# Kernel tuning notes

Measured on AMD Instinct MI355X. Metric: run time of the kernel, lower is better.

The kernel has to match this reference:

```python
import jax, jax.numpy as jnp
import numpy as np

HEAD_DEPTH = 64
CLIP = 10.0
SCALE = float(np.sqrt(HEAD_DEPTH))


def setup_inputs() -> dict:
    key = jax.random.key(0)
    kq, kk, kv, km = jax.random.split(key, 4)
    B, H, S, D = 4, 16, 2048, HEAD_DEPTH
    q = jax.random.normal(kq, (B, H, S, D), dtype=jnp.float32)
    k = jax.random.normal(kk, (B, H, S, D), dtype=jnp.float32)
    v = jax.random.normal(kv, (B, H, S, D), dtype=jnp.float32)
    # mask: (batch, n_nodes, 1) bool; True => key position is masked out
    mask = jax.random.randint(km, (B, S, 1), 0, 2).astype(bool)
    return {"q": q, "k": k, "v": v, "mask": mask}


def reference(q, k, v, mask):
    # logits: (B, H, Sq, Sk)
    logits = jnp.einsum('bhqd,bhkd->bhqk', q, k) / SCALE
    logits = CLIP * jnp.tanh(logits)  # tanh-clip of logits
    # mask (B, N, 1) -> broadcast over heads and query positions: (B, 1, 1, N)
    key_mask = mask[:, None, None, :, 0]
    logits = jnp.where(key_mask, -jnp.inf, logits)
    probs = jax.nn.softmax(logits, axis=-1)
    return jnp.einsum('bhqk,bhkd->bhqd', probs, v)
```

## Files before the change

### kernel.cpp

```cpp
#include <hip/hip_runtime.h>

typedef short bf16x8 __attribute__((ext_vector_type(8), may_alias));
typedef float f32x4 __attribute__((ext_vector_type(4)));
typedef unsigned int u32x4a __attribute__((ext_vector_type(4), may_alias));
typedef unsigned int u32x2a __attribute__((ext_vector_type(2), may_alias));
typedef unsigned short ushort;
typedef unsigned int uint;

#define B_N 4
#define H_N 16
#define S_N 2048
#define D_N 64
#define BQ 128
#define WQ 32
#define KT 64
#define NW 4
#define NBLK (B_N*H_N*(S_N/BQ))
#define TILE_BYTES 32768
#define MAXTILE (S_N/KT)
#define IMG_OFF 32768
#define WS_NEED ((size_t)IMG_OFF + (size_t)B_N*H_N*MAXTILE*TILE_BYTES)

#define MFMA16 __builtin_amdgcn_mfma_f32_16x16x32_bf16

__device__ __forceinline__ uint f2bf(float x){
  uint u = __float_as_uint(x);
  u += 0x7fffu + ((u >> 16) & 1u);
  return u >> 16;
}
__device__ __forceinline__ float bf2f(uint h){
  return __uint_as_float(h << 16);
}
__device__ __forceinline__ int ldsw(int off, int row){
  return off ^ ((row & 7) << 4);
}
__device__ __forceinline__ void gload16(const void* g, void* l){
  __builtin_amdgcn_global_load_lds((const uint __attribute__((address_space(1)))*)g,
                                   (uint __attribute__((address_space(3)))*)l, 16, 0, 0);
}

__global__ __launch_bounds__(256)
void compact_k(const int* __restrict__ Mg, int* __restrict__ cnt_ws,
               ushort* __restrict__ idx_ws)
{
  __shared__ int sws[NW];
  const int b = blockIdx.x;
  const int tid = threadIdx.x, lane = tid & 63, w = tid >> 6;
  const int* mb = Mg + (size_t)b * S_N;
  int kept[8]; int cl = 0; int base = tid * 8;
  #pragma unroll
  for (int i = 0; i < 8; ++i){ kept[i] = (mb[base+i] == 0); cl += kept[i]; }
  int inc = cl;
  #pragma unroll
  for (int d = 1; d < 64; d <<= 1){
    int o = __shfl_up(inc, d);
    if (lane >= d) inc += o;
  }
  if (lane == 63) sws[w] = inc;
  __syncthreads();
  int s0 = sws[0], s1 = sws[1], s2 = sws[2], s3 = sws[3];
  int wo = (w > 0 ? s0 : 0) + (w > 1 ? s1 : 0) + (w > 2 ? s2 : 0);
  int pos = wo + inc - cl;
  #pragma unroll
  for (int i = 0; i < 8; ++i){
    if (kept[i]) idx_ws[b*S_N + pos++] = (ushort)(base + i);
  }
  if (tid == 0) cnt_ws[b] = s0 + s1 + s2 + s3;
}

__global__ __launch_bounds__(256)
void stage_k(const float* __restrict__ Kg, const float* __restrict__ Vg,
             const int* __restrict__ cnt_ws, const ushort* __restrict__ idx_ws,
             char* __restrict__ img)
{
  __shared__ float Vl[64*65];
  const int bid = blockIdx.x;
  const int bh = bid >> 5;
  const int tile = bid & 31;
  const int b = bh >> 4;
  const int cnt = cnt_ws[b];
  const int ntile = (cnt + 63) >> 6;
  if (tile >= ntile) return;
  const int tid = threadIdx.x;
  char* G = img + (size_t)bid * TILE_BYTES;

  const int jrow = tid >> 2, c4 = tid & 3;
  int kk = tile*64 + jrow; if (kk >= cnt) kk = cnt - 1;
  const int sidx = idx_ws[b*S_N + kk];
  const size_t kvbase = (size_t)bh * (size_t)(S_N*D_N);
  const int sw = (jrow & 7) << 4;
  {
    const float4* Kp = (const float4*)(Kg + kvbase + (size_t)sidx*D_N) + c4*4;
    float4 k0 = Kp[0], k1 = Kp[1], k2 = Kp[2], k3 = Kp[3];
    float kv[16] = {k0.x,k0.y,k0.z,k0.w,k1.x,k1.y,k1.z,k1.w,
                    k2.x,k2.y,k2.z,k2.w,k3.x,k3.y,k3.z,k3.w};
    uint h[16], l[16];
    #pragma unroll
    for (int e = 0; e < 16; ++e){
      uint hh = f2bf(kv[e]); h[e] = hh; l[e] = f2bf(kv[e] - bf2f(hh));
    }
    char* r0 = G + jrow*128;
    char* r1 = G + 8192 + jrow*128;
    *(u32x4a*)(r0 + ((c4*32)      ^ sw)) = (u32x4a){h[0]|(h[1]<<16),  h[2]|(h[3]<<16),
                                                    h[4]|(h[5]<<16),  h[6]|(h[7]<<16)};
    *(u32x4a*)(r0 + ((c4*32 + 16) ^ sw)) = (u32x4a){h[8]|(h[9]<<16),  h[10]|(h[11]<<16),
                                                    h[12]|(h[13]<<16),h[14]|(h[15]<<16)};
    *(u32x4a*)(r1 + ((c4*32)      ^ sw)) = (u32x4a){l[0]|(l[1]<<16),  l[2]|(l[3]<<16),
                                                    l[4]|(l[5]<<16),  l[6]|(l[7]<<16)};
    *(u32x4a*)(r1 + ((c4*32 + 16) ^ sw)) = (u32x4a){l[8]|(l[9]<<16),  l[10]|(l[11]<<16),
                                                    l[12]|(l[13]<<16),l[14]|(l[15]<<16)};
  }
  {
    const float4* Vp = (const float4*)(Vg + kvbase + (size_t)sidx*D_N) + c4*4;
    float4 v0 = Vp[0], v1 = Vp[1], v2 = Vp[2], v3 = Vp[3];
    float vv[16] = {v0.x,v0.y,v0.z,v0.w,v1.x,v1.y,v1.z,v1.w,
                    v2.x,v2.y,v2.z,v2.w,v3.x,v3.y,v3.z,v3.w};
    #pragma unroll
    for (int e = 0; e < 16; ++e) Vl[jrow*65 + c4*16 + e] = vv[e];
  }
  __syncthreads();
  #pragma unroll
  for (int t = 0; t < 2; ++t){
    int idx2 = tid + t*256;
    int d = idx2 >> 3, g = idx2 & 7;
    int jb = (g ^ (d & 7)) * 8;
    uint hh[8], ll[8];
    #pragma unroll
    for (int e = 0; e < 8; ++e){
      float x = Vl[(jb+e)*65 + d];
      uint h = f2bf(x); hh[e] = h; ll[e] = f2bf(x - bf2f(h));
    }
    *(u32x4a*)(G + 16384 + d*128 + g*16) =
        (u32x4a){hh[0]|(hh[1]<<16), hh[2]|(hh[3]<<16), hh[4]|(hh[5]<<16), hh[6]|(hh[7]<<16)};
    *(u32x4a*)(G + 24576 + d*128 + g*16) =
        (u32x4a){ll[0]|(ll[1]<<16), ll[2]|(ll[3]<<16), ll[4]|(ll[5]<<16), ll[6]|(ll[7]<<16)};
  }
}

__global__ __launch_bounds__(256, 2)
void attn4_k(const float* __restrict__ Qg, const char* __restrict__ img,
             const int* __restrict__ cnt_ws, float* __restrict__ Og)
{
  __shared__ __align__(16) char smem[2][16384];
  __shared__ __align__(16) ushort Pb[NW][2][512];

  const int tid  = threadIdx.x;
  const int lane = tid & 63;
  const int w    = tid >> 6;
  const int c    = lane & 15;
  const int gi   = lane >> 4;

  int bid = blockIdx.x;
  int wg  = (bid & 7) * (NBLK/8) + (bid >> 3);
  int qt  = wg & 15;
  int bh  = wg >> 4;
  int b   = bh >> 4;

  const int cnt = cnt_ws[b];
  const int nhalf = (cnt + 31) >> 5;
  const char* Gb = img + (size_t)bh * MAXTILE * TILE_BYTES;

  auto stage = [&](int hidx, int sb){
    const char* T = Gb + (size_t)(hidx >> 1) * TILE_BYTES;
    const int h = hidx & 1;
    char* Bse = (char*)&smem[sb][0];
    if (w < 2){
      const char* src = T + w*8192 + h*4096 + lane*16;
      char* dst = Bse + w*4096;
      #pragma unroll
      for (int i = 0; i < 4; ++i) gload16(src + i*1024, dst + i*1024);
    } else {
      const int hl = w - 2;
      const char* base = T + 16384 + hl*8192;
      char* dst = Bse + 8192 + hl*4096;
      #pragma unroll
      for (int i = 0; i < 4; ++i){
        int pos = i*1024 + lane*16;
        int d = pos >> 6, p = (pos >> 4) & 3;
        int sd4 = (d & 3) ^ ((d >> 2) & 3);
        int G = (h*4 + (p ^ sd4)) ^ (d & 7);
        gload16(base + d*128 + G*16, dst + i*1024);
      }
    }
  };

  if (nhalf > 0) stage(0, 0);

  const int q0w = qt * BQ + w * WQ;
  bf16x8 qh[2][2], ql[2][2];
  {
    const float* Qbase = Qg + (size_t)bh * S_N * D_N;
    #pragma unroll
    for (int qs = 0; qs < 2; ++qs){
      const float* qr = Qbase + (size_t)(q0w + qs*16 + c) * D_N;
      #pragma unroll
      for (int ks = 0; ks < 2; ++ks){
        const float4* p4 = (const float4*)(qr + ks*32 + gi*8);
        float4 x0 = p4[0], x1 = p4[1];
        float xs[8] = {x0.x,x0.y,x0.z,x0.w,x1.x,x1.y,x1.z,x1.w};
        union { bf16x8 v; ushort u[8]; } uh, ul;
        #pragma unroll
        for (int e = 0; e < 8; ++e){
          uint h = f2bf(xs[e]);
          uh.u[e] = (ushort)h;
          ul.u[e] = (ushort)f2bf(xs[e] - bf2f(h));
        }
        qh[qs][ks] = uh.v; ql[qs][ks] = ul.v;
      }
    }
  }

  f32x4 Oa[2][4];
  #pragma unroll
  for (int i = 0; i < 2; ++i)
    #pragma unroll
    for (int jj = 0; jj < 4; ++jj)
      Oa[i][jj] = (f32x4){0.f,0.f,0.f,0.f};
  float zz[2] = {0.f, 0.f};

  char* PhB = (char*)&Pb[w][0][0];
  char* PlB = (char*)&Pb[w][1][0];
  const int swc16 = (c & 7) << 4;
  const int swc8  = (c & 7) << 3;
  const int e0 = (gi*16) ^ swc16;
  const int e1 = (64 + gi*16) ^ swc16;
  const int po0 = (gi*16) ^ swc8;
  const int po1 = (gi*16 + 8) ^ swc8;
  const int vsw = ((c & 3) ^ ((c >> 2) & 3));
  const int va  = (gi ^ vsw) << 4;

  __syncthreads();

  for (int tb = 0; tb < nhalf; ++tb){
    const int buf = tb & 1;
    if (tb + 1 < nhalf) stage(tb + 1, buf ^ 1);
    const char* Khi  = &smem[buf][0];
    const char* Klo  = Khi + 4096;
    const char* VThi = Khi + 8192;
    const char* VTlo = Khi + 12288;
    const bool lastt = (tb == nhalf - 1);

    #pragma unroll
    for (int qs = 0; qs < 2; ++qs){
      #pragma unroll
      for (int kt = 0; kt < 2; ++kt){
        int row = kt*16 + c;
        const char* krh = Khi + row*128;
        const char* krl = Klo + row*128;
        bf16x8 kh0 = *(const bf16x8*)(krh + e0);
        bf16x8 kh1 = *(const bf16x8*)(krh + e1);
        bf16x8 kl0 = *(const bf16x8*)(krl + e0);
        bf16x8 kl1 = *(const bf16x8*)(krl + e1);
        f32x4 s = (f32x4){0.f,0.f,0.f,0.f};
        s = MFMA16(kh0, qh[qs][0], s, 0,0,0);
        s = MFMA16(kh1, qh[qs][1], s, 0,0,0);
        s = MFMA16(kh0, ql[qs][0], s, 0,0,0);
        s = MFMA16(kh1, ql[qs][1], s, 0,0,0);
        s = MFMA16(kl0, qh[qs][0], s, 0,0,0);
        s = MFMA16(kl1, qh[qs][1], s, 0,0,0);
        float pv[4];
        #pragma unroll
        for (int r = 0; r < 4; ++r){
          float t  = __builtin_amdgcn_exp2f(s[r] * 0.3606737602222409f);
          float wv = __builtin_amdgcn_rcpf(t + 1.0f);
          pv[r] = __builtin_amdgcn_exp2f(-28.853900817779268f * wv);
        }
        if (lastt){
          int kg0 = tb*32 + kt*16 + gi*4;
          #pragma unroll
          for (int r = 0; r < 4; ++r) if (kg0 + r >= cnt) pv[r] = 0.f;
        }
        zz[qs] += (pv[0] + pv[1]) + (pv[2] + pv[3]);
        uint hA, hB, lA, lB;
        asm("v_cvt_pk_bf16_f32 %0, %1, %2" : "=v"(hA) : "v"(pv[0]), "v"(pv[1]));
        asm("v_cvt_pk_bf16_f32 %0, %1, %2" : "=v"(hB) : "v"(pv[2]), "v"(pv[3]));
        float l0 = pv[0] - __uint_as_float(hA << 16);
        float l1 = pv[1] - __uint_as_float(hA & 0xffff0000u);
        float l2 = pv[2] - __uint_as_float(hB << 16);
        float l3 = pv[3] - __uint_as_float(hB & 0xffff0000u);
        asm("v_cvt_pk_bf16_f32 %0, %1, %2" : "=v"(lA) : "v"(l0), "v"(l1));
        asm("v_cvt_pk_bf16_f32 %0, %1, %2" : "=v"(lB) : "v"(l2), "v"(l3));
        int ow = c*64 + ((kt*32 + gi*8) ^ swc8);
        *(u32x2a*)(PhB + ow) = (u32x2a){hA, hB};
        *(u32x2a*)(PlB + ow) = (u32x2a){lA, lB};
      }
      union PU { bf16x8 v; u32x2a g[2]; };
      PU pah, pal;
      pah.g[0] = *(const u32x2a*)(PhB + c*64 + po0);
      pah.g[1] = *(const u32x2a*)(PhB + c*64 + po1);
      pal.g[0] = *(const u32x2a*)(PlB + c*64 + po0);
      pal.g[1] = *(const u32x2a*)(PlB + c*64 + po1);
      #pragma unroll
      for (int ds = 0; ds < 4; ++ds){
        int drow = ds*16 + c;
        bf16x8 vh = *(const bf16x8*)(VThi + drow*64 + va);
        bf16x8 vl = *(const bf16x8*)(VTlo + drow*64 + va);
        f32x4 o = Oa[qs][ds];
        o = MFMA16(pah.v, vh, o, 0,0,0);
        o = MFMA16(pah.v, vl, o, 0,0,0);
        o = MFMA16(pal.v, vh, o, 0,0,0);
        Oa[qs][ds] = o;
      }
    }
    __syncthreads();
  }

  #pragma unroll
  for (int qs = 0; qs < 2; ++qs){
    float zt = zz[qs];
    zt += __shfl_xor(zt, 16);
    zt += __shfl_xor(zt, 32);
    float rz = 1.0f / zt;
    #pragma unroll
    for (int r = 0; r < 4; ++r){
      float rzq = __shfl(rz, gi*4 + r);
      size_t rowbase = ((size_t)bh * S_N + (size_t)(q0w + qs*16 + gi*4 + r)) * D_N;
      #pragma unroll
      for (int ds = 0; ds < 4; ++ds){
        Og[rowbase + ds*16 + c] = Oa[qs][ds][r] * rzq;
      }
    }
  }
}

__global__ __launch_bounds__(256, 2)
void attn_k(const float* __restrict__ Qg, const float* __restrict__ Kg,
            const float* __restrict__ Vg, const int* __restrict__ Mg,
            float* __restrict__ Og)
{
  __shared__ __align__(16) ushort Khi[KT*D_N];
  __shared__ __align__(16) ushort Klo[KT*D_N];
  __shared__ __align__(16) ushort Vhi[D_N*72];
  __shared__ __align__(16) ushort Vlo[D_N*72];
  __shared__ __align__(16) ushort Phl[NW*16*72];
  __shared__ __align__(16) ushort Pll[NW*16*72];
  __shared__ ushort idx_l[S_N];
  __shared__ int scan_ws[NW];

  const int tid  = threadIdx.x;
  const int lane = tid & 63;
  const int w    = tid >> 6;
  const int c    = lane & 15;
  const int gi   = lane >> 4;

  int bid = blockIdx.x;
  int wg  = (bid & 7) * (NBLK/8) + (bid >> 3);
  int qt  = wg & 15;
  int bh  = wg >> 4;
  int b   = bh >> 4;

  int cnt;
  {
    const int* mb = Mg + (size_t)b * S_N;
    int kept[8]; int cl = 0;
    int base = tid * 8;
    #pragma unroll
    for (int i = 0; i < 8; ++i){ kept[i] = (mb[base+i] == 0); cl += kept[i]; }
    int inc = cl;
    #pragma unroll
    for (int d = 1; d < 64; d <<= 1){
      int o = __shfl_up(inc, d);
      if (lane >= d) inc += o;
    }
    if (lane == 63) scan_ws[w] = inc;
    __syncthreads();
    int s0 = scan_ws[0], s1 = scan_ws[1], s2 = scan_ws[2], s3 = scan_ws[3];
    int wo = (w > 0 ? s0 : 0) + (w > 1 ? s1 : 0) + (w > 2 ? s2 : 0);
    cnt = s0 + s1 + s2 + s3;
    int pos = wo + inc - cl;
    #pragma unroll
    for (int i = 0; i < 8; ++i){
      if (kept[i]) idx_l[pos++] = (ushort)(base + i);
    }
    __syncthreads();
  }

  const int q0w = qt * BQ + w * WQ;
  bf16x8 qh[2][2], ql[2][2];
  {
    const float* Qbase = Qg + (size_t)bh * S_N * D_N;
    #pragma unroll
    for (int qs = 0; qs < 2; ++qs){
      const float* qr = Qbase + (size_t)(q0w + qs*16 + c) * D_N;
      #pragma unroll
      for (int ks = 0; ks < 2; ++ks){
        const float4* p4 = (const float4*)(qr + ks*32 + gi*8);
        float4 x0 = p4[0], x1 = p4[1];
        float xs[8] = {x0.x,x0.y,x0.z,x0.w,x1.x,x1.y,x1.z,x1.w};
        union { bf16x8 v; ushort u[8]; } uh, ul;
        #pragma unroll
        for (int e = 0; e < 8; ++e){
          uint h = f2bf(xs[e]);
          uh.u[e] = (ushort)h;
          ul.u[e] = (ushort)f2bf(xs[e] - bf2f(h));
        }
        qh[qs][ks] = uh.v; ql[qs][ks] = ul.v;
      }
    }
  }

  f32x4 Oa[2][4];
  #pragma unroll
  for (int i = 0; i < 2; ++i)
    #pragma unroll
    for (int jj = 0; jj < 4; ++jj)
      Oa[i][jj] = (f32x4){0.f,0.f,0.f,0.f};
  float zz[2] = {0.f, 0.f};

  ushort* Ph = Phl + w * (16*72);
  ushort* Pl = Pll + w * (16*72);

  const int jrow = tid >> 2;
  const int c4   = tid & 3;
  const size_t kvbase = (size_t)bh * S_N * D_N;

  const int ntile = (cnt + KT - 1) >> 6;
  for (int tb = 0; tb < ntile; ++tb){
    {
      int kk = tb*KT + jrow;
      int ci = kk < cnt ? kk : cnt - 1;
      int sidx = idx_l[ci];
      const float4* Kp = (const float4*)(Kg + kvbase + (size_t)sidx * D_N) + c4*4;
      const float4* Vp = (const float4*)(Vg + kvbase + (size_t)sidx * D_N) + c4*4;
      float4 k0 = Kp[0], k1 = Kp[1], k2 = Kp[2], k3 = Kp[3];
      float kv[16] = {k0.x,k0.y,k0.z,k0.w,k1.x,k1.y,k1.z,k1.w,
                      k2.x,k2.y,k2.z,k2.w,k3.x,k3.y,k3.z,k3.w};
      uint kh[16], klv[16];
      #pragma unroll
      for (int e = 0; e < 16; ++e){
        uint h = f2bf(kv[e]);
        kh[e] = h; klv[e] = f2bf(kv[e] - bf2f(h));
      }
      u32x4a H0 = (u32x4a){kh[0]|(kh[1]<<16),   kh[2]|(kh[3]<<16),
                           kh[4]|(kh[5]<<16),   kh[6]|(kh[7]<<16)};
      u32x4a H1 = (u32x4a){kh[8]|(kh[9]<<16),   kh[10]|(kh[11]<<16),
                           kh[12]|(kh[13]<<16), kh[14]|(kh[15]<<16)};
      u32x4a L0 = (u32x4a){klv[0]|(klv[1]<<16),   klv[2]|(klv[3]<<16),
                           klv[4]|(klv[5]<<16),   klv[6]|(klv[7]<<16)};
      u32x4a L1 = (u32x4a){klv[8]|(klv[9]<<16),   klv[10]|(klv[11]<<16),
                           klv[12]|(klv[13]<<16), klv[14]|(klv[15]<<16)};
      char* krh = (char*)Khi + jrow*128;
      char* krl = (char*)Klo + jrow*128;
      int o0 = ldsw(c4*32, jrow), o1 = ldsw(c4*32 + 16, jrow);
      *(u32x4a*)(krh + o0) = H0;  *(u32x4a*)(krh + o1) = H1;
      *(u32x4a*)(krl + o0) = L0;  *(u32x4a*)(krl + o1) = L1;

      float4 v0 = Vp[0], v1 = Vp[1], v2 = Vp[2], v3 = Vp[3];
      float vv[16] = {v0.x,v0.y,v0.z,v0.w,v1.x,v1.y,v1.z,v1.w,
                      v2.x,v2.y,v2.z,v2.w,v3.x,v3.y,v3.z,v3.w};
      #pragma unroll
      for (int e = 0; e < 16; ++e){
        int d = c4*16 + e;
        uint h  = f2bf(vv[e]);
        uint l2 = f2bf(vv[e] - bf2f(h));
        int off = d*144 + ldsw(jrow*2, d);
        *(ushort*)((char*)Vhi + off) = (ushort)h;
        *(ushort*)((char*)Vlo + off) = (ushort)l2;
      }
    }
    __syncthreads();

    const bool lastt = (tb == ntile - 1);
    #pragma unroll
    for (int qs = 0; qs < 2; ++qs){
      #pragma unroll
      for (int kt = 0; kt < 4; ++kt){
        int row = kt*16 + c;
        const char* krh = (const char*)Khi + row*128;
        const char* krl = (const char*)Klo + row*128;
        int e0 = ldsw(16*gi, row), e1 = ldsw(64 + 16*gi, row);
        bf16x8 kh0 = *(const bf16x8*)(krh + e0);
        bf16x8 kh1 = *(const bf16x8*)(krh + e1);
        bf16x8 kl0 = *(const bf16x8*)(krl + e0);
        bf16x8 kl1 = *(const bf16x8*)(krl + e1);
        f32x4 s = (f32x4){0.f,0.f,0.f,0.f};
        s = MFMA16(kh0, qh[qs][0], s, 0,0,0);
        s = MFMA16(kh1, qh[qs][1], s, 0,0,0);
        s = MFMA16(kh0, ql[qs][0], s, 0,0,0);
        s = MFMA16(kh1, ql[qs][1], s, 0,0,0);
        s = MFMA16(kl0, qh[qs][0], s, 0,0,0);
        s = MFMA16(kl1, qh[qs][1], s, 0,0,0);
        float pv[4];
        #pragma unroll
        for (int r = 0; r < 4; ++r){
          float t  = __builtin_amdgcn_exp2f(s[r] * 0.3606737602222409f);
          float wv = __builtin_amdgcn_rcpf(t + 1.0f);
          pv[r] = __builtin_amdgcn_exp2f(-28.853900817779268f * wv);
        }
        if (lastt){
          int kg0 = tb*KT + kt*16 + gi*4;
          #pragma unroll
          for (int r = 0; r < 4; ++r) if (kg0 + r >= cnt) pv[r] = 0.f;
        }
        zz[qs] += (pv[0] + pv[1]) + (pv[2] + pv[3]);
        uint h0 = f2bf(pv[0]), h1 = f2bf(pv[1]),
             h2 = f2bf(pv[2]), h3 = f2bf(pv[3]);
        uint l0 = f2bf(pv[0]-bf2f(h0)), l1 = f2bf(pv[1]-bf2f(h1)),
             l2 = f2bf(pv[2]-bf2f(h2)), l3 = f2bf(pv[3]-bf2f(h3));
        int ow = c*144 + ldsw(kt*32 + gi*8, c);
        *(u32x2a*)((char*)Ph + ow) = (u32x2a){h0|(h1<<16), h2|(h3<<16)};
        *(u32x2a*)((char*)Pl + ow) = (u32x2a){l0|(l1<<16), l2|(l3<<16)};
      }
      bf16x8 pah[2], pal[2];
      {
        const char* prh = (const char*)Ph + c*144;
        const char* prl = (const char*)Pl + c*144;
        #pragma unroll
        for (int ks = 0; ks < 2; ++ks){
          int oo = ldsw(64*ks + 16*gi, c);
          pah[ks] = *(const bf16x8*)(prh + oo);
          pal[ks] = *(const bf16x8*)(prl + oo);
        }
      }
      #pragma unroll
      for (int ds = 0; ds < 4; ++ds){
        int drow = ds*16 + c;
        const char* vrh = (const char*)Vhi + drow*144;
        const char* vrl = (const char*)Vlo + drow*144;
        f32x4 o = Oa[qs][ds];
        #pragma unroll
        for (int ks = 0; ks < 2; ++ks){
          int oo = ldsw(64*ks + 16*gi, drow);
          bf16x8 vh = *(const bf16x8*)(vrh + oo);
          bf16x8 vl = *(const bf16x8*)(vrl + oo);
          o = MFMA16(pah[ks], vh, o, 0,0,0);
          o = MFMA16(pah[ks], vl, o, 0,0,0);
          o = MFMA16(pal[ks], vh, o, 0,0,0);
        }
        Oa[qs][ds] = o;
      }
    }
    __syncthreads();
  }

  #pragma unroll
  for (int qs = 0; qs < 2; ++qs){
    float zt = zz[qs];
    zt += __shfl_xor(zt, 16);
    zt += __shfl_xor(zt, 32);
    float rz = 1.0f / zt;
    #pragma unroll
    for (int r = 0; r < 4; ++r){
      float rzq = __shfl(rz, gi*4 + r);
      size_t rowbase = ((size_t)bh * S_N + (size_t)(q0w + qs*16 + gi*4 + r)) * D_N;
      #pragma unroll
      for (int ds = 0; ds < 4; ++ds){
        Og[rowbase + ds*16 + c] = Oa[qs][ds][r] * rzq;
      }
    }
  }
}

extern "C" void kernel_launch(void* const* d_in, const int* in_sizes, int n_in,
                              void* d_out, int out_size, void* d_ws, size_t ws_size,
                              hipStream_t stream) {
  const float* Qg = (const float*)d_in[0];
  const float* Kg = (const float*)d_in[1];
  const float* Vg = (const float*)d_in[2];
  const int*   Mg = (const int*)d_in[3];
  float* Og = (float*)d_out;
  if (ws_size >= WS_NEED){
    int*    cnt_ws = (int*)d_ws;
    ushort* idx_ws = (ushort*)((char*)d_ws + 64);
    char*   img    = (char*)d_ws + IMG_OFF;
    compact_k<<<dim3(B_N), dim3(256), 0, stream>>>(Mg, cnt_ws, idx_ws);
    stage_k<<<dim3(B_N*H_N*MAXTILE), dim3(256), 0, stream>>>(Kg, Vg, cnt_ws, idx_ws, img);
    attn4_k<<<dim3(NBLK), dim3(256), 0, stream>>>(Qg, img, cnt_ws, Og);
  } else {
    attn_k<<<dim3(NBLK), dim3(256), 0, stream>>>(Qg, Kg, Vg, Mg, Og);
  }
}
```

Measured before the change: 157.1 us.

## Keep softmax probabilities in registers by permuting V layout to match MFMA output

The V transpose image in the staging kernel is reordered so that the key index permutation matches the MFMA accumulator layout. The attention kernel can then feed the packed bf16 probabilities straight from registers as the A operand of the PV MFMA, skipping the per-warp LDS round trip for P. The loops are also reordered so K fragments load once for both query subtiles and V fragments load once for both. The cost is more live registers, which could pressure occupancy at two blocks per CU, and the V swizzle is dropped, which may bring back LDS bank conflicts.

```diff
diff --git a/kernel.cpp b/kernel.cpp
--- a/kernel.cpp
+++ b/kernel.cpp
@@ -122,27 +122,29 @@
   #pragma unroll
   for (int t = 0; t < 2; ++t){
     int idx2 = tid + t*256;
-    int d = idx2 >> 3, g = idx2 & 7;
-    int jb = (g ^ (d & 7)) * 8;
+    int d = idx2 >> 3;
+    int h = (idx2 >> 2) & 1;
+    int g = idx2 & 3;
+    int kb = h*32 + g*4;
     uint hh[8], ll[8];
     #pragma unroll
     for (int e = 0; e < 8; ++e){
-      float x = Vl[(jb+e)*65 + d];
-      uint h = f2bf(x); hh[e] = h; ll[e] = f2bf(x - bf2f(h));
-    }
-    *(u32x4a*)(G + 16384 + d*128 + g*16) =
+      int k = kb + (e & 3) + ((e >> 2) << 4);
+      float x = Vl[k*65 + d];
+      uint hv = f2bf(x); hh[e] = hv; ll[e] = f2bf(x - bf2f(hv));
+    }
+    *(u32x4a*)(G + 16384 + d*128 + h*64 + g*16) =
         (u32x4a){hh[0]|(hh[1]<<16), hh[2]|(hh[3]<<16), hh[4]|(hh[5]<<16), hh[6]|(hh[7]<<16)};
-    *(u32x4a*)(G + 24576 + d*128 + g*16) =
+    *(u32x4a*)(G + 24576 + d*128 + h*64 + g*16) =
         (u32x4a){ll[0]|(ll[1]<<16), ll[2]|(ll[3]<<16), ll[4]|(ll[5]<<16), ll[6]|(ll[7]<<16)};
   }
 }
 
 __global__ __launch_bounds__(256, 2)
-void attn4_k(const float* __restrict__ Qg, const char* __restrict__ img,
+void attn5_k(const float* __restrict__ Qg, const char* __restrict__ img,
              const int* __restrict__ cnt_ws, float* __restrict__ Og)
 {
   __shared__ __align__(16) char smem[2][16384];
-  __shared__ __align__(16) ushort Pb[NW][2][512];
 
   const int tid  = threadIdx.x;
   const int lane = tid & 63;
@@ -171,15 +173,14 @@
       for (int i = 0; i < 4; ++i) gload16(src + i*1024, dst + i*1024);
     } else {
       const int hl = w - 2;
-      const char* base = T + 16384 + hl*8192;
+      const char* base = T + 16384 + hl*8192 + h*64;
       char* dst = Bse + 8192 + hl*4096;
       #pragma unroll
       for (int i = 0; i < 4; ++i){
         int pos = i*1024 + lane*16;
-        int d = pos >> 6, p = (pos >> 4) & 3;
-        int sd4 = (d & 3) ^ ((d >> 2) & 3);
-        int G = (h*4 + (p ^ sd4)) ^ (d & 7);
-        gload16(base + d*128 + G*16, dst + i*1024);
+        int d = pos >> 6;
+        int g = (pos >> 4) & 3;
+        gload16(base + d*128 + g*16, dst + i*1024);
       }
     }
   };
@@ -218,16 +219,9 @@
       Oa[i][jj] = (f32x4){0.f,0.f,0.f,0.f};
   float zz[2] = {0.f, 0.f};
 
-  char* PhB = (char*)&Pb[w][0][0];
-  char* PlB = (char*)&Pb[w][1][0];
   const int swc16 = (c & 7) << 4;
-  const int swc8  = (c & 7) << 3;
   const int e0 = (gi*16) ^ swc16;
   const int e1 = (64 + gi*16) ^ swc16;
-  const int po0 = (gi*16) ^ swc8;
-  const int po1 = (gi*16 + 8) ^ swc8;
-  const int vsw = ((c & 3) ^ ((c >> 2) & 3));
-  const int va  = (gi ^ vsw) << 4;
 
   __syncthreads();
 
@@ -240,17 +234,18 @@
     const char* VTlo = Khi + 12288;
     const bool lastt = (tb == nhalf - 1);
 
-    #pragma unroll
-    for (int qs = 0; qs < 2; ++qs){
-      #pragma unroll
-      for (int kt = 0; kt < 2; ++kt){
-        int row = kt*16 + c;
-        const char* krh = Khi + row*128;
-        const char* krl = Klo + row*128;
-        bf16x8 kh0 = *(const bf16x8*)(krh + e0);
-        bf16x8 kh1 = *(const bf16x8*)(krh + e1);
-        bf16x8 kl0 = *(const bf16x8*)(krl + e0);
-        bf16x8 kl1 = *(const bf16x8*)(krl + e1);
+    uint sH[2][4], sL[2][4];
+    #pragma unroll
+    for (int kt = 0; kt < 2; ++kt){
+      int row = kt*16 + c;
+      const char* krh = Khi + row*128;
+      const char* krl = Klo + row*128;
+      bf16x8 kh0 = *(const bf16x8*)(krh + e0);
+      bf16x8 kh1 = *(const bf16x8*)(krh + e1);
+      bf16x8 kl0 = *(const bf16x8*)(krl + e0);
+      bf16x8 kl1 = *(const bf16x8*)(krl + e1);
+      #pragma unroll
+      for (int qs = 0; qs < 2; ++qs){
         f32x4 s = (f32x4){0.f,0.f,0.f,0.f};
         s = MFMA16(kh0, qh[qs][0], s, 0,0,0);
         s = MFMA16(kh1, qh[qs][1], s, 0,0,0);
@@ -280,25 +275,28 @@
         float l3 = pv[3] - __uint_as_float(hB & 0xffff0000u);
         asm("v_cvt_pk_bf16_f32 %0, %1, %2" : "=v"(lA) : "v"(l0), "v"(l1));
         asm("v_cvt_pk_bf16_f32 %0, %1, %2" : "=v"(lB) : "v"(l2), "v"(l3));
-        int ow = c*64 + ((kt*32 + gi*8) ^ swc8);
-        *(u32x2a*)(PhB + ow) = (u32x2a){hA, hB};
-        *(u32x2a*)(PlB + ow) = (u32x2a){lA, lB};
-      }
-      union PU { bf16x8 v; u32x2a g[2]; };
-      PU pah, pal;
-      pah.g[0] = *(const u32x2a*)(PhB + c*64 + po0);
-      pah.g[1] = *(const u32x2a*)(PhB + c*64 + po1);
-      pal.g[0] = *(const u32x2a*)(PlB + c*64 + po0);
-      pal.g[1] = *(const u32x2a*)(PlB + c*64 + po1);
-      #pragma unroll
-      for (int ds = 0; ds < 4; ++ds){
-        int drow = ds*16 + c;
-        bf16x8 vh = *(const bf16x8*)(VThi + drow*64 + va);
-        bf16x8 vl = *(const bf16x8*)(VTlo + drow*64 + va);
+        sH[qs][kt*2+0] = hA; sH[qs][kt*2+1] = hB;
+        sL[qs][kt*2+0] = lA; sL[qs][kt*2+1] = lB;
+      }
+    }
+    union PU { u32x4a g; bf16x8 v; };
+    PU pah[2], pal[2];
+    #pragma unroll
+    for (int qs = 0; qs < 2; ++qs){
+      pah[qs].g = (u32x4a){sH[qs][0], sH[qs][1], sH[qs][2], sH[qs][3]};
+      pal[qs].g = (u32x4a){sL[qs][0], sL[qs][1], sL[qs][2], sL[qs][3]};
+    }
+    #pragma unroll
+    for (int ds = 0; ds < 4; ++ds){
+      int drow = ds*16 + c;
+      bf16x8 vh = *(const bf16x8*)(VThi + drow*64 + gi*16);
+      bf16x8 vl = *(const bf16x8*)(VTlo + drow*64 + gi*16);
+      #pragma unroll
+      for (int qs = 0; qs < 2; ++qs){
         f32x4 o = Oa[qs][ds];
-        o = MFMA16(pah.v, vh, o, 0,0,0);
-        o = MFMA16(pah.v, vl, o, 0,0,0);
-        o = MFMA16(pal.v, vh, o, 0,0,0);
+        o = MFMA16(pah[qs].v, vh, o, 0,0,0);
+        o = MFMA16(pah[qs].v, vl, o, 0,0,0);
+        o = MFMA16(pal[qs].v, vh, o, 0,0,0);
         Oa[qs][ds] = o;
       }
     }
@@ -565,7 +563,7 @@
     char*   img    = (char*)d_ws + IMG_OFF;
     compact_k<<<dim3(B_N), dim3(256), 0, stream>>>(Mg, cnt_ws, idx_ws);
     stage_k<<<dim3(B_N*H_N*MAXTILE), dim3(256), 0, stream>>>(Kg, Vg, cnt_ws, idx_ws, img);
-    attn4_k<<<dim3(NBLK), dim3(256), 0, stream>>>(Qg, img, cnt_ws, Og);
+    attn5_k<<<dim3(NBLK), dim3(256), 0, stream>>>(Qg, img, cnt_ws, Og);
   } else {
     attn_k<<<dim3(NBLK), dim3(256), 0, stream>>>(Qg, Kg, Vg, Mg, Og);
   }
```

Result: faster. 137.2 us (-12.7%).
